# Optimization experiments

Hardware: AMD Instinct MI355X
Metric: run time of the kernel (lower is better)

## Reference

```python
import jax, jax.numpy as jnp
import numpy as np

EPS = 1e-12


def setup_inputs() -> dict:
    key = jax.random.key(0)
    k1, k2 = jax.random.split(key)
    ide_feats = jax.random.normal(k1, (4096, 256), dtype=jnp.float32)
    u_feats = jax.random.normal(k2, (16384, 256), dtype=jnp.float32)
    return {"ide_feats": ide_feats, "u_feats": u_feats}


def reference(ide_feats, u_feats):
    # euclidean_dist: sqrt(sum((x_i - y_j)^2) + eps) -> [N, M]
    # computed via the GEMM expansion to avoid the [N, M, D] intermediate
    x2 = jnp.sum(ide_feats * ide_feats, axis=-1)[:, None]   # [N, 1]
    y2 = jnp.sum(u_feats * u_feats, axis=-1)[None, :]       # [1, M]
    xy = jnp.einsum('nd,md->nm', ide_feats, u_feats)        # [N, M]
    d2 = jnp.maximum(x2 + y2 - 2.0 * xy, 0.0)
    dists = jnp.sqrt(d2 + EPS)                              # [N, M]
    d = jnp.mean(dists, axis=-1)                            # [N]
    # dist_loss: sum_{i,j} sqrt((d_i - d_j)^2 + eps)
    diff = d[:, None] - d[None, :]                          # [N, N]
    loss = jnp.sum(jnp.sqrt(diff * diff + EPS))
    return loss
```

## Files before the change

kernel.cpp:

```cpp
#include <hip/hip_runtime.h>
#include <hip/hip_bf16.h>
#include <cstdint>

#define N_IDE 4096
#define M_U   16384
#define D_DIM 256
#define EPSF  1e-12f
#define INV_M (1.0f / 16384.0f)

typedef _Float16 f16x8 __attribute__((ext_vector_type(8)));
typedef float    f32x4 __attribute__((ext_vector_type(4)));

__device__ __forceinline__ void gll16(const void* g, void* l) {
  __builtin_amdgcn_global_load_lds(
      (const __attribute__((address_space(1))) void*)(uintptr_t)g,
      (__attribute__((address_space(3))) void*)(uint32_t)(uintptr_t)l,
      16, 0, 0);
}

__device__ __forceinline__ unsigned short f2h_bits(float f) {
  _Float16 h = (_Float16)f;
  return __builtin_bit_cast(unsigned short, h);
}

__global__ __launch_bounds__(256) void k_conv(const float* __restrict__ ide,
                                              const float* __restrict__ u,
                                              unsigned short* __restrict__ Ah,
                                              unsigned short* __restrict__ Bh,
                                              float* __restrict__ x2,
                                              float* __restrict__ y2) {
  int gw = (blockIdx.x * 256 + threadIdx.x) >> 6;
  int l  = threadIdx.x & 63;
  const float4* src;
  ushort4* dst;
  float* nrm;
  if (gw < N_IDE) {
    src = (const float4*)(ide + (size_t)gw * D_DIM);
    dst = (ushort4*)(Ah + (size_t)gw * D_DIM);
    nrm = x2 + gw;
  } else {
    int r = gw - N_IDE;
    src = (const float4*)(u + (size_t)r * D_DIM);
    dst = (ushort4*)(Bh + (size_t)r * D_DIM);
    nrm = y2 + r;
  }
  float4 v = src[l];
  float s = v.x * v.x + v.y * v.y + v.z * v.z + v.w * v.w;
  ushort4 o;
  o.x = f2h_bits(v.x); o.y = f2h_bits(v.y);
  o.z = f2h_bits(v.z); o.w = f2h_bits(v.w);
  dst[l] = o;
#pragma unroll
  for (int m = 1; m <= 32; m <<= 1) s += __shfl_xor(s, m, 64);
  if (l == 0) *nrm = s;
}

__global__ __launch_bounds__(512, 2) void k_gemm(const unsigned short* __restrict__ Ah,
                                                 const unsigned short* __restrict__ Bh,
                                                 const float* __restrict__ x2,
                                                 const float* __restrict__ y2,
                                                 float* __restrict__ partial) {
  __shared__ __align__(16) unsigned short sA[128 * 256];
  __shared__ float rowacc[8][128];

  const int t    = threadIdx.x;
  const int w    = t >> 6;
  const int l    = t & 63;
  const int lrow = l & 15;
  const int lhi  = l >> 4;
  const int bx   = blockIdx.x;
  const int by   = blockIdx.y;

#pragma unroll
  for (int i = 0; i < 8; ++i) {
    int L = i * 512 + t;
    int row = L >> 5;
    int p = L & 31;
    int c = (p & 24) | ((p & 7) ^ (row & 7));
    gll16(Ah + (size_t)(by * 128 + row) * D_DIM + c * 8,
          sA + (size_t)(i * 512 + w * 64) * 8);
  }
  __syncthreads();

  const int colbase = bx * 512 + w * 64;

  const unsigned short* bptr[4];
#pragma unroll
  for (int nj = 0; nj < 4; ++nj)
    bptr[nj] = Bh + (size_t)(colbase + nj * 16 + lrow) * D_DIM + lhi * 8;

  f32x4 acc[8][4];
#pragma unroll
  for (int mi = 0; mi < 8; ++mi)
#pragma unroll
    for (int nj = 0; nj < 4; ++nj)
      acc[mi][nj] = (f32x4){0.f, 0.f, 0.f, 0.f};

  f16x8 bfb[2][4];
#pragma unroll
  for (int nj = 0; nj < 4; ++nj) bfb[0][nj] = *(const f16x8*)(bptr[nj]);

#pragma unroll
  for (int kt = 0; kt < 8; ++kt) {
    if (kt < 7) {
#pragma unroll
      for (int nj = 0; nj < 4; ++nj)
        bfb[(kt + 1) & 1][nj] = *(const f16x8*)(bptr[nj] + (kt + 1) * 32);
    }
    const int lc = kt * 4 + lhi;
    const int pc = (lc & 24) | ((lc & 7) ^ (lrow & 7));
    f16x8 af[8];
#pragma unroll
    for (int mi = 0; mi < 8; ++mi)
      af[mi] = *(const f16x8*)(sA + (size_t)(mi * 16 + lrow) * 256 + pc * 8);
#pragma unroll
    for (int mi = 0; mi < 8; ++mi)
#pragma unroll
      for (int nj = 0; nj < 4; ++nj)
        acc[mi][nj] = __builtin_amdgcn_mfma_f32_16x16x32_f16(af[mi], bfb[kt & 1][nj],
                                                             acc[mi][nj], 0, 0, 0);
  }

  float yv[4];
#pragma unroll
  for (int nj = 0; nj < 4; ++nj) yv[nj] = y2[colbase + nj * 16 + lrow];

#pragma unroll
  for (int mi = 0; mi < 8; ++mi) {
    float4 x2v = *(const float4*)&x2[by * 128 + mi * 16 + lhi * 4];
    float xr[4] = {x2v.x, x2v.y, x2v.z, x2v.w};
    float rv[4];
#pragma unroll
    for (int rr = 0; rr < 4; ++rr) {
      float ssum = 0.f;
#pragma unroll
      for (int nj = 0; nj < 4; ++nj) {
        float d2 = xr[rr] + yv[nj] - 2.0f * acc[mi][nj][rr];
        d2 = fmaxf(d2, 0.0f);
        ssum += __builtin_amdgcn_sqrtf(d2 + EPSF);
      }
      ssum += __shfl_xor(ssum, 1, 64);
      ssum += __shfl_xor(ssum, 2, 64);
      ssum += __shfl_xor(ssum, 4, 64);
      ssum += __shfl_xor(ssum, 8, 64);
      rv[rr] = ssum;
    }
    if (lrow == 0)
      *(float4*)&rowacc[w][mi * 16 + lhi * 4] = make_float4(rv[0], rv[1], rv[2], rv[3]);
  }

  __syncthreads();
  if (t < 128) {
    float s = 0.f;
#pragma unroll
    for (int ww = 0; ww < 8; ++ww) s += rowacc[ww][t];
    partial[(size_t)bx * N_IDE + by * 128 + t] = s;
  }
}

__global__ __launch_bounds__(256) void k_dsum(const float* __restrict__ partial,
                                              float* __restrict__ d) {
  int k = blockIdx.x * 256 + threadIdx.x;
  float s = 0.f;
#pragma unroll
  for (int b = 0; b < 32; ++b) s += partial[(size_t)b * N_IDE + k];
  d[k] = s;
}

__global__ __launch_bounds__(256) void k_loss(const float* __restrict__ d,
                                              float* __restrict__ out) {
  __shared__ float sd[N_IDE];
  __shared__ float wsum[4];
  int t = threadIdx.x;
  for (int k = t; k < N_IDE; k += 256) sd[k] = d[k];
  __syncthreads();
  int tid = blockIdx.x * 256 + t;
  int i   = tid >> 4;
  int jl  = tid & 15;
  float di = sd[i];
  float s  = 0.f;
  for (int k = 0; k < 256; ++k) {
    float diff = (di - sd[jl + k * 16]) * INV_M;
    s += __builtin_amdgcn_sqrtf(diff * diff + EPSF);
  }
#pragma unroll
  for (int m = 1; m <= 32; m <<= 1) s += __shfl_xor(s, m, 64);
  if ((t & 63) == 0) wsum[t >> 6] = s;
  __syncthreads();
  if (t == 0) atomicAdd(out, wsum[0] + wsum[1] + wsum[2] + wsum[3]);
}

extern "C" void kernel_launch(void* const* d_in, const int* in_sizes, int n_in,
                              void* d_out, int out_size, void* d_ws, size_t ws_size,
                              hipStream_t stream) {
  (void)in_sizes; (void)n_in; (void)out_size; (void)ws_size;
  const float* ide = (const float*)d_in[0];
  const float* u   = (const float*)d_in[1];
  float* out = (float*)d_out;

  char* ws = (char*)d_ws;
  size_t off = 0;
  unsigned short* Ah = (unsigned short*)(ws + off); off += (size_t)N_IDE * D_DIM * 2;
  unsigned short* Bh = (unsigned short*)(ws + off); off += (size_t)M_U  * D_DIM * 2;
  float* x2      = (float*)(ws + off); off += (size_t)N_IDE * 4;
  float* y2      = (float*)(ws + off); off += (size_t)M_U * 4;
  float* partial = (float*)(ws + off); off += (size_t)32 * N_IDE * 4;
  float* dvec    = (float*)(ws + off); off += (size_t)N_IDE * 4;

  hipMemsetAsync(d_out, 0, sizeof(float), stream);
  k_conv<<<(N_IDE + M_U) / 4, 256, 0, stream>>>(ide, u, Ah, Bh, x2, y2);
  k_gemm<<<dim3(32, 32), 512, 0, stream>>>(Ah, Bh, x2, y2, partial);
  k_dsum<<<N_IDE / 256, 256, 0, stream>>>(partial, dvec);
  k_loss<<<256, 256, 0, stream>>>(dvec, out);
}
```

Before: 141.2 us.

## Restructure GEMM into 256x256 tiles with double-buffered LDS A/B pipeline

```diff
diff --git a/kernel.cpp b/kernel.cpp
--- a/kernel.cpp
+++ b/kernel.cpp
@@ -22,6 +22,8 @@
   _Float16 h = (_Float16)f;
   return __builtin_bit_cast(unsigned short, h);
 }
+
+#define SBAR()  asm volatile("s_barrier" ::: "memory")
 
 __global__ __launch_bounds__(256) void k_conv(const float* __restrict__ ide,
                                               const float* __restrict__ u,
@@ -60,34 +62,47 @@
                                                  const float* __restrict__ x2,
                                                  const float* __restrict__ y2,
                                                  float* __restrict__ partial) {
-  __shared__ __align__(16) unsigned short sA[128 * 256];
-  __shared__ float rowacc[8][128];
+  __shared__ __align__(16) unsigned short sA[2][16384];
+  __shared__ __align__(16) unsigned short sB[2][16384];
+  __shared__ float rowacc[4][256];
 
   const int t    = threadIdx.x;
   const int w    = t >> 6;
   const int l    = t & 63;
   const int lrow = l & 15;
   const int lhi  = l >> 4;
-  const int bx   = blockIdx.x;
-  const int by   = blockIdx.y;
-
-#pragma unroll
-  for (int i = 0; i < 8; ++i) {
-    int L = i * 512 + t;
-    int row = L >> 5;
-    int p = L & 31;
-    int c = (p & 24) | ((p & 7) ^ (row & 7));
-    gll16(Ah + (size_t)(by * 128 + row) * D_DIM + c * 8,
-          sA + (size_t)(i * 512 + w * 64) * 8);
-  }
-  __syncthreads();
-
-  const int colbase = bx * 512 + w * 64;
-
-  const unsigned short* bptr[4];
-#pragma unroll
-  for (int nj = 0; nj < 4; ++nj)
-    bptr[nj] = Bh + (size_t)(colbase + nj * 16 + lrow) * D_DIM + lhi * 8;
+  const int wm   = w >> 2, wn = w & 3;
+  const int bn   = blockIdx.x;
+  const int bm   = blockIdx.y;
+
+  const int sr  = t >> 3;
+  const int skc = (t & 7) ^ (sr & 7);
+  const size_t soff = (size_t)sr * D_DIM + (size_t)skc * 8;
+
+  const unsigned short* Abase = Ah + (size_t)bm * 256 * D_DIM;
+  const unsigned short* Bbase = Bh + (size_t)bn * 256 * D_DIM;
+
+  auto stA = [&](int k1, int h) {
+    const unsigned short* src = Abase + (size_t)h * 128 * D_DIM + k1 * 64 + soff;
+    unsigned short* dst = &sA[k1 & 1][h * 8192 + w * 512];
+    gll16(src, dst);
+    gll16(src + 64 * D_DIM, dst + 4096);
+  };
+  auto stB = [&](int k1, int h) {
+    const unsigned short* src = Bbase + (size_t)h * 128 * D_DIM + k1 * 64 + soff;
+    unsigned short* dst = &sB[k1 & 1][h * 8192 + w * 512];
+    gll16(src, dst);
+    gll16(src + 64 * D_DIM, dst + 4096);
+  };
+
+  stA(0, 0); stA(0, 1);
+  stB(0, 0); stB(0, 1);
+  stB(1, 0); stB(1, 1);
+  asm volatile("s_waitcnt vmcnt(4)" ::: "memory");
+  SBAR();
+
+  const int sl0 = ((lhi)     ^ (lrow & 7)) * 8;
+  const int sl1 = ((lhi + 4) ^ (lrow & 7)) * 8;
 
   f32x4 acc[8][4];
 #pragma unroll
@@ -96,38 +111,88 @@
     for (int nj = 0; nj < 4; ++nj)
       acc[mi][nj] = (f32x4){0.f, 0.f, 0.f, 0.f};
 
-  f16x8 bfb[2][4];
-#pragma unroll
-  for (int nj = 0; nj < 4; ++nj) bfb[0][nj] = *(const f16x8*)(bptr[nj]);
-
-#pragma unroll
-  for (int kt = 0; kt < 8; ++kt) {
-    if (kt < 7) {
-#pragma unroll
-      for (int nj = 0; nj < 4; ++nj)
-        bfb[(kt + 1) & 1][nj] = *(const f16x8*)(bptr[nj] + (kt + 1) * 32);
+#pragma unroll
+  for (int kt = 0; kt < 4; ++kt) {
+    const unsigned short* Ab = &sA[kt & 1][wm * 8192 + lrow * 64];
+    const unsigned short* Bb = &sB[kt & 1][(wn >> 1) * 8192 + ((wn & 1) * 64 + lrow) * 64];
+    f16x8 bf[4][2], af[4];
+
+#pragma unroll
+    for (int nj = 0; nj < 4; ++nj) {
+      bf[nj][0] = *(const f16x8*)(Bb + nj * 1024 + sl0);
+      bf[nj][1] = *(const f16x8*)(Bb + nj * 1024 + sl1);
     }
-    const int lc = kt * 4 + lhi;
-    const int pc = (lc & 24) | ((lc & 7) ^ (lrow & 7));
-    f16x8 af[8];
-#pragma unroll
-    for (int mi = 0; mi < 8; ++mi)
-      af[mi] = *(const f16x8*)(sA + (size_t)(mi * 16 + lrow) * 256 + pc * 8);
-#pragma unroll
-    for (int mi = 0; mi < 8; ++mi)
-#pragma unroll
-      for (int nj = 0; nj < 4; ++nj)
-        acc[mi][nj] = __builtin_amdgcn_mfma_f32_16x16x32_f16(af[mi], bfb[kt & 1][nj],
+#pragma unroll
+    for (int mi = 0; mi < 4; ++mi)
+      af[mi] = *(const f16x8*)(Ab + mi * 1024 + sl0);
+    if (kt < 3) stA(kt + 1, 0);
+    SBAR();
+    __builtin_amdgcn_s_setprio(1);
+#pragma unroll
+    for (int mi = 0; mi < 4; ++mi)
+#pragma unroll
+      for (int nj = 0; nj < 4; ++nj)
+        acc[mi][nj] = __builtin_amdgcn_mfma_f32_16x16x32_f16(af[mi], bf[nj][0],
                                                              acc[mi][nj], 0, 0, 0);
+    __builtin_amdgcn_s_setprio(0);
+    SBAR();
+
+#pragma unroll
+    for (int mi = 0; mi < 4; ++mi)
+      af[mi] = *(const f16x8*)(Ab + (64 + mi * 16) * 64 + sl0);
+    if (kt < 3) stA(kt + 1, 1);
+    SBAR();
+    __builtin_amdgcn_s_setprio(1);
+#pragma unroll
+    for (int mi = 0; mi < 4; ++mi)
+#pragma unroll
+      for (int nj = 0; nj < 4; ++nj)
+        acc[4 + mi][nj] = __builtin_amdgcn_mfma_f32_16x16x32_f16(af[mi], bf[nj][0],
+                                                                 acc[4 + mi][nj], 0, 0, 0);
+    __builtin_amdgcn_s_setprio(0);
+    SBAR();
+
+#pragma unroll
+    for (int mi = 0; mi < 4; ++mi)
+      af[mi] = *(const f16x8*)(Ab + mi * 1024 + sl1);
+    if (kt < 2) stB(kt + 2, 0);
+    SBAR();
+    __builtin_amdgcn_s_setprio(1);
+#pragma unroll
+    for (int mi = 0; mi < 4; ++mi)
+#pragma unroll
+      for (int nj = 0; nj < 4; ++nj)
+        acc[mi][nj] = __builtin_amdgcn_mfma_f32_16x16x32_f16(af[mi], bf[nj][1],
+                                                             acc[mi][nj], 0, 0, 0);
+    __builtin_amdgcn_s_setprio(0);
+    SBAR();
+
+#pragma unroll
+    for (int mi = 0; mi < 4; ++mi)
+      af[mi] = *(const f16x8*)(Ab + (64 + mi * 16) * 64 + sl1);
+    if (kt < 2) stB(kt + 2, 1);
+    SBAR();
+    __builtin_amdgcn_s_setprio(1);
+#pragma unroll
+    for (int mi = 0; mi < 4; ++mi)
+#pragma unroll
+      for (int nj = 0; nj < 4; ++nj)
+        acc[4 + mi][nj] = __builtin_amdgcn_mfma_f32_16x16x32_f16(af[mi], bf[nj][1],
+                                                                 acc[4 + mi][nj], 0, 0, 0);
+    __builtin_amdgcn_s_setprio(0);
+    if (kt < 2)       asm volatile("s_waitcnt vmcnt(4)" ::: "memory");
+    else if (kt == 2) asm volatile("s_waitcnt vmcnt(0)" ::: "memory");
+    SBAR();
   }
 
   float yv[4];
 #pragma unroll
-  for (int nj = 0; nj < 4; ++nj) yv[nj] = y2[colbase + nj * 16 + lrow];
+  for (int nj = 0; nj < 4; ++nj)
+    yv[nj] = y2[bn * 256 + wn * 64 + nj * 16 + lrow];
 
 #pragma unroll
   for (int mi = 0; mi < 8; ++mi) {
-    float4 x2v = *(const float4*)&x2[by * 128 + mi * 16 + lhi * 4];
+    float4 x2v = *(const float4*)&x2[bm * 256 + wm * 128 + mi * 16 + lhi * 4];
     float xr[4] = {x2v.x, x2v.y, x2v.z, x2v.w};
     float rv[4];
 #pragma unroll
@@ -146,16 +211,14 @@
       rv[rr] = ssum;
     }
     if (lrow == 0)
-      *(float4*)&rowacc[w][mi * 16 + lhi * 4] = make_float4(rv[0], rv[1], rv[2], rv[3]);
+      *(float4*)&rowacc[wn][wm * 128 + mi * 16 + lhi * 4] =
+          make_float4(rv[0], rv[1], rv[2], rv[3]);
   }
 
   __syncthreads();
-  if (t < 128) {
-    float s = 0.f;
-#pragma unroll
-    for (int ww = 0; ww < 8; ++ww) s += rowacc[ww][t];
-    partial[(size_t)bx * N_IDE + by * 128 + t] = s;
-  }
+  if (t < 256)
+    partial[(size_t)bn * N_IDE + bm * 256 + t] =
+        rowacc[0][t] + rowacc[1][t] + rowacc[2][t] + rowacc[3][t];
 }
 
 __global__ __launch_bounds__(256) void k_dsum(const float* __restrict__ partial,
@@ -163,7 +226,7 @@
   int k = blockIdx.x * 256 + threadIdx.x;
   float s = 0.f;
 #pragma unroll
-  for (int b = 0; b < 32; ++b) s += partial[(size_t)b * N_IDE + k];
+  for (int b = 0; b < 64; ++b) s += partial[(size_t)b * N_IDE + k];
   d[k] = s;
 }
 
@@ -204,12 +267,12 @@
   unsigned short* Bh = (unsigned short*)(ws + off); off += (size_t)M_U  * D_DIM * 2;
   float* x2      = (float*)(ws + off); off += (size_t)N_IDE * 4;
   float* y2      = (float*)(ws + off); off += (size_t)M_U * 4;
-  float* partial = (float*)(ws + off); off += (size_t)32 * N_IDE * 4;
+  float* partial = (float*)(ws + off); off += (size_t)64 * N_IDE * 4;
   float* dvec    = (float*)(ws + off); off += (size_t)N_IDE * 4;
 
   hipMemsetAsync(d_out, 0, sizeof(float), stream);
   k_conv<<<(N_IDE + M_U) / 4, 256, 0, stream>>>(ide, u, Ah, Bh, x2, y2);
-  k_gemm<<<dim3(32, 32), 512, 0, stream>>>(Ah, Bh, x2, y2, partial);
+  k_gemm<<<dim3(64, 16), 512, 0, stream>>>(Ah, Bh, x2, y2, partial);
   k_dsum<<<N_IDE / 256, 256, 0, stream>>>(partial, dvec);
   k_loss<<<256, 256, 0, stream>>>(dvec, out);
 }
```

After: 152.0 us. 7.7% more time.
